# Kernel optimization log

Hardware: AMD Instinct MI355X
Metric: run time of the kernel (lower is better)

Reference implementation:

```python
import jax, jax.numpy as jnp
import numpy as np
import math

C = 256
GROUPS = 8
EPS = 1e-5

def setup_inputs() -> dict:
    key = jax.random.key(0)
    ks = jax.random.split(key, 10)
    b, c, h, w = 4, C, 64, 64
    x = jax.random.normal(ks[0], (b, c, h, w), dtype=jnp.float32)
    scale = 1.0 / math.sqrt(c)
    wq = jax.random.normal(ks[1], (c, c), dtype=jnp.float32) * scale
    wk = jax.random.normal(ks[2], (c, c), dtype=jnp.float32) * scale
    wv = jax.random.normal(ks[3], (c, c), dtype=jnp.float32) * scale
    wp = jax.random.normal(ks[4], (c, c), dtype=jnp.float32) * scale
    bq = jnp.zeros((c,), jnp.float32)
    bk = jnp.zeros((c,), jnp.float32)
    bv = jnp.zeros((c,), jnp.float32)
    bp = jnp.zeros((c,), jnp.float32)
    gamma = jnp.ones((c,), jnp.float32)
    beta = jnp.zeros((c,), jnp.float32)
    return {"x": x, "gamma": gamma, "beta": beta, "wq": wq, "bq": bq,
            "wk": wk, "bk": bk, "wv": wv, "bv": bv, "wp": wp, "bp": bp}

def _group_norm(x, gamma, beta):
    b, c, h, w = x.shape
    xr = x.reshape(b, GROUPS, c // GROUPS, h, w)
    mean = xr.mean(axis=(2, 3, 4), keepdims=True)
    var = xr.var(axis=(2, 3, 4), keepdims=True)
    xn = ((xr - mean) * jax.lax.rsqrt(var + EPS)).reshape(b, c, h, w)
    return xn * gamma[None, :, None, None] + beta[None, :, None, None]

def _conv1x1(x, w, bias):
    # 1x1 conv == channel matmul: [b,c,h,w] x [out,in] -> [b,out,h,w]
    return jnp.einsum('bchw,dc->bdhw', x, w) + bias[None, :, None, None]

def reference(x, gamma, beta, wq, bq, wk, bk, wv, bv, wp, bp):
    b, c, h, w = x.shape
    residual = x
    xn = _group_norm(x, gamma, beta)
    q = _conv1x1(xn, wq, bq).reshape(b, c, h * w).transpose(0, 2, 1)  # [b, hw, c]
    k = _conv1x1(xn, wk, bk).reshape(b, c, h * w)                    # [b, c, hw]
    v = _conv1x1(xn, wv, bv).reshape(b, c, h * w).transpose(0, 2, 1)  # [b, hw, c]
    attn = jnp.einsum('bqc,bck->bqk', q, k) / jnp.sqrt(jnp.float32(c))
    attn = jax.nn.softmax(attn, axis=-1)
    out = jnp.einsum('bqk,bkc->bqc', attn, v)                         # [b, hw, c]
    out = out.transpose(0, 2, 1).reshape(b, c, h, w)
    out = _conv1x1(out, wp, bp)
    return out + residual
```

## Files before the change

### kernel.cpp

```cpp
#include <hip/hip_runtime.h>

#define HW 4096
#define CD 256
#define KB 32
#define NKB 64
#define NSP 2
#define C1 0.09016844f

typedef __bf16 bf16x8v __attribute__((ext_vector_type(8)));
typedef float f32x4 __attribute__((ext_vector_type(4)));
typedef unsigned short u16;
typedef unsigned int u32;
typedef u16 u16x4 __attribute__((ext_vector_type(4)));
typedef u16 u16x8 __attribute__((ext_vector_type(8)));

static __device__ __forceinline__ u16 f2bf(float f){
  __bf16 h = (__bf16)f;
  return __builtin_bit_cast(u16, h);
}
static __device__ __forceinline__ float bf2f(u16 v){
  u32 u = ((u32)v) << 16;
  return __builtin_bit_cast(float, u);
}

static __device__ __forceinline__ f32x4 MFMA(u16x8 a, u16x8 b, f32x4 c){
  return __builtin_amdgcn_mfma_f32_16x16x32_bf16(
      __builtin_bit_cast(bf16x8v, a), __builtin_bit_cast(bf16x8v, b), c, 0, 0, 0);
}

#define GLL16(gsrc, ldst) __builtin_amdgcn_global_load_lds( \
    (const __attribute__((address_space(1))) void*)(gsrc),  \
    (__attribute__((address_space(3))) void*)(ldst), 16, 0, 0)

__global__ void k_prep(const float* __restrict__ wq, const float* __restrict__ wk,
                       const float* __restrict__ wv, const float* __restrict__ wp,
                       u16* __restrict__ Wbf){
  int z = blockIdx.y;
  const float* src = (z==0)?wq:(z==1)?wk:(z==2)?wv:wp;
  int i = (blockIdx.x*256 + threadIdx.x)*4;
  float4 v = *(const float4*)(src + i);
  u16x4 o = { f2bf(v.x), f2bf(v.y), f2bf(v.z), f2bf(v.w) };
  *(u16x4*)(Wbf + z*65536 + i) = o;
}

__global__ void k_gn1(const float* __restrict__ x, float* __restrict__ gpart){
  int g = blockIdx.x, b = blockIdx.y, ck = blockIdx.z;
  int tid = threadIdx.x;
  const float* xp = x + ((size_t)(b*CD) + g*32)*HW + ck*512;
  float s0 = 0.f, s1 = 0.f;
  #pragma unroll
  for (int j = 0; j < 16; ++j){
    int idx = j*1024 + tid*4;
    float4 v = *(const float4*)(xp + (size_t)(idx >> 9)*HW + (idx & 511));
    s0 += v.x + v.y + v.z + v.w;
    s1 += v.x*v.x + v.y*v.y + v.z*v.z + v.w*v.w;
  }
  #pragma unroll
  for (int m = 1; m < 64; m <<= 1){ s0 += __shfl_xor(s0, m); s1 += __shfl_xor(s1, m); }
  __shared__ float red[8];
  int lane = tid & 63, wave = tid >> 6;
  if (lane == 0){ red[wave] = s0; red[4+wave] = s1; }
  __syncthreads();
  if (tid == 0){
    float* dst = gpart + ((b*8 + g)*8 + ck)*2;
    dst[0] = red[0]+red[1]+red[2]+red[3];
    dst[1] = red[4]+red[5]+red[6]+red[7];
  }
}

__global__ void k_gn2(const float* __restrict__ x, const float* __restrict__ gamma,
                      const float* __restrict__ beta, const float* __restrict__ gpart,
                      u16* __restrict__ xnT){
  int g = blockIdx.x, b = blockIdx.y, ck = blockIdx.z;
  int tid = threadIdx.x;
  float s0 = 0.f, s1 = 0.f;
  #pragma unroll
  for (int s = 0; s < 8; ++s){
    const float* p = gpart + ((b*8 + g)*8 + s)*2;
    s0 += p[0]; s1 += p[1];
  }
  float inv_n = 1.0f/(32.0f*HW);
  float mean = s0*inv_n;
  float var = s1*inv_n - mean*mean;
  float rstd = rsqrtf(var + 1e-5f);
  int pl = tid >> 2, c8 = (tid & 3)*8;
  float av[8], bv_[8];
  #pragma unroll
  for (int e = 0; e < 8; ++e){
    int c = g*32 + c8 + e;
    float a = rstd * gamma[c];
    av[e] = a;
    bv_[e] = beta[c] - mean*a;
  }
  const float* xb = x + (size_t)(b*CD + g*32 + c8)*HW;
  #pragma unroll
  for (int it = 0; it < 8; ++it){
    int p = ck*512 + it*64 + pl;
    u16x8 o;
    #pragma unroll
    for (int e = 0; e < 8; ++e){
      float v = xb[(size_t)e*HW + p];
      o[e] = f2bf(v*av[e] + bv_[e]);
    }
    *(u16x8*)(xnT + ((size_t)(b*HW) + p)*CD + g*32 + c8) = o;
  }
}

__global__ __launch_bounds__(256,2) void k_qkv(const u16* __restrict__ xnT, const u16* __restrict__ Wbf,
    const float* __restrict__ bq, const float* __restrict__ bk, const float* __restrict__ bv,
    u16* __restrict__ Q, u16* __restrict__ K, u16* __restrict__ V){
  __shared__ u16 tile[4][4096];
  int z = blockIdx.z, b = blockIdx.y, pbase = blockIdx.x*64;
  int tid = threadIdx.x, lane = tid & 63, wave = tid >> 6;
  int lq = lane & 15, lg = lane >> 4;
  const u16* W = Wbf + z*65536;
  const float* bias = (z==0)?bq:(z==1)?bk:bv;
  int nbase = wave*64;
  f32x4 acc[4][4] = {};
  #pragma unroll
  for (int kk = 0; kk < 8; ++kk){
    u16x8 af[4], bf[4];
    #pragma unroll
    for (int m = 0; m < 4; ++m)
      af[m] = *(const u16x8*)(xnT + ((size_t)(b*HW + pbase + m*16 + lq))*CD + kk*32 + lg*8);
    #pragma unroll
    for (int n = 0; n < 4; ++n)
      bf[n] = *(const u16x8*)(W + (size_t)(nbase + n*16 + lq)*CD + kk*32 + lg*8);
    #pragma unroll
    for (int m = 0; m < 4; ++m)
      #pragma unroll
      for (int n = 0; n < 4; ++n)
        acc[m][n] = MFMA(af[m], bf[n], acc[m][n]);
  }
  #pragma unroll
  for (int n = 0; n < 4; ++n){
    float bb = bias[nbase + n*16 + lq];
    #pragma unroll
    for (int m = 0; m < 4; ++m){
      acc[m][n][0] += bb; acc[m][n][1] += bb; acc[m][n][2] += bb; acc[m][n][3] += bb;
    }
  }
  if (z == 2){
    #pragma unroll
    for (int m = 0; m < 4; ++m)
      #pragma unroll
      for (int n = 0; n < 4; ++n){
        int d = nbase + n*16 + lq;
        int p0 = pbase + m*16 + lg*4;
        u16x4 o = { f2bf(acc[m][n][0]), f2bf(acc[m][n][1]), f2bf(acc[m][n][2]), f2bf(acc[m][n][3]) };
        *(u16x4*)(V + (size_t)(b*CD + d)*HW + p0) = o;
      }
  } else {
    u16* dst = (z==0)?Q:K;
    u16* tl = tile[wave];
    #pragma unroll
    for (int m = 0; m < 4; ++m)
      #pragma unroll
      for (int n = 0; n < 4; ++n)
        #pragma unroll
        for (int r = 0; r < 4; ++r){
          int row = m*16 + lg*4 + r;
          int col = n*16 + lq;
          tl[row*64 + ((((col>>3) + row) & 7)<<3) + (col & 7)] = f2bf(acc[m][n][r]);
        }
    #pragma unroll
    for (int j = 0; j < 8; ++j){
      int idx = j*64 + lane;
      int row = idx >> 3, ch = idx & 7;
      u16x8 v = *(const u16x8*)(tl + row*64 + (((ch + row)&7)<<3));
      *(u16x8*)(dst + ((size_t)(b*HW + pbase + row))*CD + nbase + ch*8) = v;
    }
  }
}

__global__ __launch_bounds__(512,4) void k_attn(const u16* __restrict__ Q, const u16* __restrict__ K,
    const u16* __restrict__ V, u16* __restrict__ Opart, float2* __restrict__ ml){
  extern __shared__ char smem[];
  int tid = threadIdx.x, lane = tid & 63, wave = tid >> 6;
  int lq = lane & 15, lg = lane >> 4;
  int pair = wave >> 1, half = wave & 1;
  int qt = blockIdx.x, sp = blockIdx.y, b = blockIdx.z;
  int qbase = qt*64 + pair*16;
  int key0 = sp*(NKB*KB);

  int ke[2], ve[2];
  #pragma unroll
  for (int i = 0; i < 2; ++i){
    int G = i*512 + tid;
    int kr = G >> 5;
    ke[i] = kr*CD + (((G & 31) ^ kr) & 31)*8;
    int vrow = G >> 3;
    int p = (G >> 2) & 1;
    int j = ((G & 3) - vrow) & 3;
    ve[i] = (vrow*2 + p)*HW + j*8;
  }
  int bvo = (lq>>1)*128 + (((lq&1)*4 + ((lg + (lq>>1)) & 3)))*16;

  u16x8 qa[8];
  #pragma unroll
  for (int cc = 0; cc < 8; ++cc)
    qa[cc] = *(const u16x8*)(Q + ((size_t)(b*HW + qbase + lq))*CD + cc*32 + lg*8);

  f32x4 o[8] = {};
  float m_ = 0.f, l_ = 0.f;

  const u16* Kb = K + (size_t)(b*HW + key0)*CD;
  const u16* Vb = V + (size_t)(b*CD)*HW + key0;
  char* Pw = smem + 65536 + pair*1024;
  float* mb = (float*)(smem + 69632);

  {
    char* kd = smem; char* vd = smem + 32768;
    #pragma unroll
    for (int i = 0; i < 2; ++i){
      GLL16(Kb + ke[i], kd + i*8192 + wave*1024);
      GLL16(Vb + ve[i], vd + i*8192 + wave*1024);
    }
  }
  __syncthreads();
  int cur = 0;
  for (int kb = 0; kb < NKB; ++kb){
    if (kb + 1 < NKB){
      char* kd = smem + (cur^1)*16384;
      const u16* kg = Kb + (size_t)(kb+1)*KB*CD;
      #pragma unroll
      for (int i = 0; i < 2; ++i)
        GLL16(kg + ke[i], kd + i*8192 + wave*1024);
    }
    const char* kt = smem + cur*16384;

    f32x4 sa = (f32x4){0.f,0.f,0.f,0.f};
    int row = half*16 + lq;
    #pragma unroll
    for (int cc = 0; cc < 8; ++cc){
      int ch = cc*4 + lg;
      u16x8 kf = *(const u16x8*)(kt + row*512 + (((ch ^ row) & 31) << 4));
      sa = MFMA(kf, qa[cc], sa);
    }
    float t0 = sa[0]*C1, t1 = sa[1]*C1, t2 = sa[2]*C1, t3 = sa[3]*C1;
    float v = fmaxf(fmaxf(t0, t1), fmaxf(t2, t3));
    v = fmaxf(v, __shfl_xor(v, 16));
    v = fmaxf(v, __shfl_xor(v, 32));
    if (lg == 0) mb[pair*32 + half*16 + lq] = v;
    float rs;
    {
      float p0 = exp2f(t0 - m_), p1 = exp2f(t1 - m_);
      float p2 = exp2f(t2 - m_), p3 = exp2f(t3 - m_);
      rs = (p0 + p1) + (p2 + p3);
      u32 w0 = (u32)f2bf(p0) | ((u32)f2bf(p1) << 16);
      u32 w1 = (u32)f2bf(p2) | ((u32)f2bf(p3) << 16);
      int chunk = 2*half + (lg>>1);
      int slot  = (chunk + (lq>>1)) & 3;
      int base  = (lq>>1)*128 + ((lq&1)*4 + slot)*16;
      *(u32*)(Pw + base + ((2*lg + 0)&3)*4) = w0;
      *(u32*)(Pw + base + ((2*lg + 1)&3)*4) = w1;
    }
    rs += __shfl_xor(rs, 16);
    rs += __shfl_xor(rs, 32);
    l_ += rs;
    if (kb + 1 < NKB){
      asm volatile("s_waitcnt vmcnt(2) lgkmcnt(0)" ::: "memory");
      __builtin_amdgcn_s_barrier();
      __builtin_amdgcn_sched_barrier(0);
      char* vd = smem + 32768 + (cur^1)*16384;
      const u16* vg = Vb + (kb+1)*KB;
      #pragma unroll
      for (int i = 0; i < 2; ++i)
        GLL16(vg + ve[i], vd + i*8192 + wave*1024);
    } else {
      __syncthreads();
    }
    float mx = fmaxf(mb[pair*32 + lq], mb[pair*32 + 16 + lq]);
    u16x8 pa = *(const u16x8*)(Pw + bvo);
    const char* vt = smem + 32768 + cur*16384;
    #pragma unroll
    for (int f = 0; f < 8; ++f){
      u16x8 vf = *(const u16x8*)(vt + (half*8 + f)*1024 + bvo);
      o[f] = MFMA(pa, vf, o[f]);
    }
    if (!__all(mx <= m_ + 8.0f)){
      float nm = fmaxf(m_, mx);
      float corr = exp2f(m_ - nm);
      m_ = nm;
      l_ *= corr;
      float cr[4];
      #pragma unroll
      for (int r = 0; r < 4; ++r)
        cr[r] = __shfl(corr, lg*4 + r);
      #pragma unroll
      for (int f = 0; f < 8; ++f)
        #pragma unroll
        for (int r = 0; r < 4; ++r)
          o[f][r] *= cr[r];
    }
    cur ^= 1;
  }
  __syncthreads();
  if (lg == 0) mb[pair*32 + half*16 + lq] = l_;
  __syncthreads();
  float l_tot = mb[pair*32 + lq] + mb[pair*32 + 16 + lq];
  size_t ob = ((size_t)((sp*4 + b)*HW + qbase))*CD;
  #pragma unroll
  for (int f = 0; f < 8; ++f){
    int c = (half*8 + f)*16 + lq;
    #pragma unroll
    for (int r = 0; r < 4; ++r)
      Opart[ob + (size_t)(lg*4 + r)*CD + c] = f2bf(o[f][r]);
  }
  if (half == 0 && lg == 0)
    ml[(size_t)(sp*4 + b)*HW + qbase + lq] = make_float2(m_, l_tot);
}

__global__ void k_comb(const u16* __restrict__ Opart, const float2* __restrict__ ml,
                       u16* __restrict__ Opm){
  int b = blockIdx.y;
  int q = blockIdx.x*8 + (threadIdx.x >> 5);
  int c0 = (threadIdx.x & 31)*8;
  float2 e[NSP];
  float m = -3.0e38f;
  #pragma unroll
  for (int s = 0; s < NSP; ++s){
    e[s] = ml[(size_t)(s*4 + b)*HW + q];
    m = fmaxf(m, e[s].x);
  }
  float w[NSP], den = 0.f;
  #pragma unroll
  for (int s = 0; s < NSP; ++s){
    w[s] = exp2f(e[s].x - m);
    den += e[s].y * w[s];
  }
  float inv = 1.0f / den;
  float sum[8] = {};
  #pragma unroll
  for (int s = 0; s < NSP; ++s){
    u16x8 v = *(const u16x8*)(Opart + ((size_t)((s*4 + b)*HW) + q)*CD + c0);
    float ws = w[s];
    #pragma unroll
    for (int t = 0; t < 8; ++t)
      sum[t] += bf2f(v[t]) * ws;
  }
  u16x8 o;
  #pragma unroll
  for (int t = 0; t < 8; ++t)
    o[t] = f2bf(sum[t]*inv);
  *(u16x8*)(Opm + ((size_t)(b*HW) + q)*CD + c0) = o;
}

__global__ __launch_bounds__(256,2) void k_proj(const u16* __restrict__ Opm, const u16* __restrict__ Wp,
    const float* __restrict__ bp, const float* __restrict__ x, float* __restrict__ out){
  int b = blockIdx.y, pbase = blockIdx.x*64;
  int tid = threadIdx.x, lane = tid & 63, wave = tid >> 6;
  int lq = lane & 15, lg = lane >> 4;
  int nbase = wave*64;
  f32x4 acc[4][4] = {};
  #pragma unroll
  for (int kk = 0; kk < 8; ++kk){
    u16x8 af[4], bf[4];
    #pragma unroll
    for (int m = 0; m < 4; ++m)
      af[m] = *(const u16x8*)(Opm + ((size_t)(b*HW + pbase + m*16 + lq))*CD + kk*32 + lg*8);
    #pragma unroll
    for (int n = 0; n < 4; ++n)
      bf[n] = *(const u16x8*)(Wp + (size_t)(nbase + n*16 + lq)*CD + kk*32 + lg*8);
    #pragma unroll
    for (int m = 0; m < 4; ++m)
      #pragma unroll
      for (int n = 0; n < 4; ++n)
        acc[m][n] = MFMA(af[m], bf[n], acc[m][n]);
  }
  #pragma unroll
  for (int m = 0; m < 4; ++m)
    #pragma unroll
    for (int n = 0; n < 4; ++n){
      int d = nbase + n*16 + lq;
      int p0 = pbase + m*16 + lg*4;
      size_t base = (size_t)(b*CD + d)*HW + p0;
      float bb = bp[d];
      float4 res = *(const float4*)(x + base);
      float4 ov;
      ov.x = acc[m][n][0] + bb + res.x;
      ov.y = acc[m][n][1] + bb + res.y;
      ov.z = acc[m][n][2] + bb + res.z;
      ov.w = acc[m][n][3] + bb + res.w;
      *(float4*)(out + base) = ov;
    }
}

extern "C" void kernel_launch(void* const* d_in, const int* in_sizes, int n_in,
                              void* d_out, int out_size, void* d_ws, size_t ws_size,
                              hipStream_t stream){
  const float* x     = (const float*)d_in[0];
  const float* gamma = (const float*)d_in[1];
  const float* beta  = (const float*)d_in[2];
  const float* wq    = (const float*)d_in[3];
  const float* bq    = (const float*)d_in[4];
  const float* wk    = (const float*)d_in[5];
  const float* bk    = (const float*)d_in[6];
  const float* wv    = (const float*)d_in[7];
  const float* bv    = (const float*)d_in[8];
  const float* wp    = (const float*)d_in[9];
  const float* bp    = (const float*)d_in[10];
  float* out = (float*)d_out;

  char* ws = (char*)d_ws;
  u16*   xnT   = (u16*)(ws);
  u16*   Qb    = (u16*)(ws + (8ull<<20));
  u16*   Kb    = (u16*)(ws + (16ull<<20));
  u16*   Vb    = (u16*)(ws + (24ull<<20));
  u16*   Opm   = (u16*)(ws + (32ull<<20));
  u16*   Wbf   = (u16*)(ws + (40ull<<20));
  float2* mlb  = (float2*)(ws + (40ull<<20) + (512ull<<10));
  u16*   Opart = (u16*)(ws + (41ull<<20));
  float* gpart = (float*)Qb;

  hipFuncSetAttribute((const void*)k_attn, hipFuncAttributeMaxDynamicSharedMemorySize, 70144);

  k_prep<<<dim3(64,4), 256, 0, stream>>>(wq, wk, wv, wp, Wbf);
  k_gn1 <<<dim3(8,4,8), 256, 0, stream>>>(x, gpart);
  k_gn2 <<<dim3(8,4,8), 256, 0, stream>>>(x, gamma, beta, gpart, xnT);
  k_qkv <<<dim3(64,4,3), 256, 0, stream>>>(xnT, Wbf, bq, bk, bv, Qb, Kb, Vb);
  k_attn<<<dim3(64,NSP,4), 512, 70144, stream>>>(Qb, Kb, Vb, Opart, mlb);
  k_comb<<<dim3(512,4), 256, 0, stream>>>(Opart, mlb, Opm);
  k_proj<<<dim3(64,4), 256, 0, stream>>>(Opm, Wbf + 3*65536, bp, x, out);
}
```

Baseline: 164.9 us.

## Fuse weight prep into GN stats, prescale Q, rebarrier attention loop, halve proj tile

The weight bf16 conversion moves into the group-norm statistics kernel, which removes one kernel launch. The softmax scale C1 is folded into Q when Q is produced, so the attention loop no longer multiplies each score. The attention loop's barriers are rearranged: an unconditional wait and barrier before the V prefetch, plus a second barrier at the end of each iteration. The projection kernel uses 32-row tiles, doubling its grid to 512 blocks so more CUs have work. The extra barrier per iteration could add stall time, and bf16 rounding of the prescaled Q changes numerics slightly.

```diff
diff --git a/kernel.cpp b/kernel.cpp
--- a/kernel.cpp
+++ b/kernel.cpp
@@ -32,20 +32,21 @@
     (const __attribute__((address_space(1))) void*)(gsrc),  \
     (__attribute__((address_space(3))) void*)(ldst), 16, 0, 0)
 
-__global__ void k_prep(const float* __restrict__ wq, const float* __restrict__ wk,
-                       const float* __restrict__ wv, const float* __restrict__ wp,
-                       u16* __restrict__ Wbf){
-  int z = blockIdx.y;
-  const float* src = (z==0)?wq:(z==1)?wk:(z==2)?wv:wp;
-  int i = (blockIdx.x*256 + threadIdx.x)*4;
-  float4 v = *(const float4*)(src + i);
-  u16x4 o = { f2bf(v.x), f2bf(v.y), f2bf(v.z), f2bf(v.w) };
-  *(u16x4*)(Wbf + z*65536 + i) = o;
-}
-
-__global__ void k_gn1(const float* __restrict__ x, float* __restrict__ gpart){
+__global__ void k_gn1(const float* __restrict__ x,
+                      const float* __restrict__ wq, const float* __restrict__ wk,
+                      const float* __restrict__ wv, const float* __restrict__ wp,
+                      u16* __restrict__ Wbf, float* __restrict__ gpart){
   int g = blockIdx.x, b = blockIdx.y, ck = blockIdx.z;
   int tid = threadIdx.x;
+  {
+    int bid = (ck*4 + b)*8 + g;
+    int i4 = bid*1024 + tid*4;
+    int z = i4 >> 16, off = i4 & 65535;
+    const float* src = (z==0)?wq:(z==1)?wk:(z==2)?wv:wp;
+    float4 v = *(const float4*)(src + off);
+    u16x4 o = { f2bf(v.x), f2bf(v.y), f2bf(v.z), f2bf(v.w) };
+    *(u16x4*)(Wbf + i4) = o;
+  }
   const float* xp = x + ((size_t)(b*CD) + g*32)*HW + ck*512;
   float s0 = 0.f, s1 = 0.f;
   #pragma unroll
@@ -115,6 +116,7 @@
   int lq = lane & 15, lg = lane >> 4;
   const u16* W = Wbf + z*65536;
   const float* bias = (z==0)?bq:(z==1)?bk:bv;
+  float scl = (z==0) ? C1 : 1.0f;
   int nbase = wave*64;
   f32x4 acc[4][4] = {};
   #pragma unroll
@@ -136,9 +138,10 @@
   for (int n = 0; n < 4; ++n){
     float bb = bias[nbase + n*16 + lq];
     #pragma unroll
-    for (int m = 0; m < 4; ++m){
-      acc[m][n][0] += bb; acc[m][n][1] += bb; acc[m][n][2] += bb; acc[m][n][3] += bb;
-    }
+    for (int m = 0; m < 4; ++m)
+      #pragma unroll
+      for (int r = 0; r < 4; ++r)
+        acc[m][n][r] = (acc[m][n][r] + bb) * scl;
   }
   if (z == 2){
     #pragma unroll
@@ -237,15 +240,14 @@
       u16x8 kf = *(const u16x8*)(kt + row*512 + (((ch ^ row) & 31) << 4));
       sa = MFMA(kf, qa[cc], sa);
     }
-    float t0 = sa[0]*C1, t1 = sa[1]*C1, t2 = sa[2]*C1, t3 = sa[3]*C1;
-    float v = fmaxf(fmaxf(t0, t1), fmaxf(t2, t3));
+    float v = fmaxf(fmaxf(sa[0], sa[1]), fmaxf(sa[2], sa[3]));
     v = fmaxf(v, __shfl_xor(v, 16));
     v = fmaxf(v, __shfl_xor(v, 32));
     if (lg == 0) mb[pair*32 + half*16 + lq] = v;
     float rs;
     {
-      float p0 = exp2f(t0 - m_), p1 = exp2f(t1 - m_);
-      float p2 = exp2f(t2 - m_), p3 = exp2f(t3 - m_);
+      float p0 = exp2f(sa[0] - m_), p1 = exp2f(sa[1] - m_);
+      float p2 = exp2f(sa[2] - m_), p3 = exp2f(sa[3] - m_);
       rs = (p0 + p1) + (p2 + p3);
       u32 w0 = (u32)f2bf(p0) | ((u32)f2bf(p1) << 16);
       u32 w1 = (u32)f2bf(p2) | ((u32)f2bf(p3) << 16);
@@ -258,17 +260,19 @@
     rs += __shfl_xor(rs, 16);
     rs += __shfl_xor(rs, 32);
     l_ += rs;
+    if (kb + 1 < NKB)
+      asm volatile("s_waitcnt vmcnt(2) lgkmcnt(0)" ::: "memory");
+    else
+      asm volatile("s_waitcnt vmcnt(0) lgkmcnt(0)" ::: "memory");
+    __builtin_amdgcn_s_barrier();
+    __builtin_amdgcn_sched_barrier(0);
+
     if (kb + 1 < NKB){
-      asm volatile("s_waitcnt vmcnt(2) lgkmcnt(0)" ::: "memory");
-      __builtin_amdgcn_s_barrier();
-      __builtin_amdgcn_sched_barrier(0);
       char* vd = smem + 32768 + (cur^1)*16384;
       const u16* vg = Vb + (kb+1)*KB;
       #pragma unroll
       for (int i = 0; i < 2; ++i)
         GLL16(vg + ve[i], vd + i*8192 + wave*1024);
-    } else {
-      __syncthreads();
     }
     float mx = fmaxf(mb[pair*32 + lq], mb[pair*32 + 16 + lq]);
     u16x8 pa = *(const u16x8*)(Pw + bvo);
@@ -292,6 +296,11 @@
         #pragma unroll
         for (int r = 0; r < 4; ++r)
           o[f][r] *= cr[r];
+    }
+    if (kb + 1 < NKB){
+      asm volatile("s_waitcnt vmcnt(2)" ::: "memory");
+      __builtin_amdgcn_s_barrier();
+      __builtin_amdgcn_sched_barrier(0);
     }
     cur ^= 1;
   }
@@ -348,28 +357,28 @@
 
 __global__ __launch_bounds__(256,2) void k_proj(const u16* __restrict__ Opm, const u16* __restrict__ Wp,
     const float* __restrict__ bp, const float* __restrict__ x, float* __restrict__ out){
-  int b = blockIdx.y, pbase = blockIdx.x*64;
+  int b = blockIdx.y, pbase = blockIdx.x*32;
   int tid = threadIdx.x, lane = tid & 63, wave = tid >> 6;
   int lq = lane & 15, lg = lane >> 4;
   int nbase = wave*64;
-  f32x4 acc[4][4] = {};
+  f32x4 acc[2][4] = {};
   #pragma unroll
   for (int kk = 0; kk < 8; ++kk){
-    u16x8 af[4], bf[4];
-    #pragma unroll
-    for (int m = 0; m < 4; ++m)
+    u16x8 af[2], bf[4];
+    #pragma unroll
+    for (int m = 0; m < 2; ++m)
       af[m] = *(const u16x8*)(Opm + ((size_t)(b*HW + pbase + m*16 + lq))*CD + kk*32 + lg*8);
     #pragma unroll
     for (int n = 0; n < 4; ++n)
       bf[n] = *(const u16x8*)(Wp + (size_t)(nbase + n*16 + lq)*CD + kk*32 + lg*8);
     #pragma unroll
-    for (int m = 0; m < 4; ++m)
+    for (int m = 0; m < 2; ++m)
       #pragma unroll
       for (int n = 0; n < 4; ++n)
         acc[m][n] = MFMA(af[m], bf[n], acc[m][n]);
   }
   #pragma unroll
-  for (int m = 0; m < 4; ++m)
+  for (int m = 0; m < 2; ++m)
     #pragma unroll
     for (int n = 0; n < 4; ++n){
       int d = nbase + n*16 + lq;
@@ -415,11 +424,10 @@
 
   hipFuncSetAttribute((const void*)k_attn, hipFuncAttributeMaxDynamicSharedMemorySize, 70144);
 
-  k_prep<<<dim3(64,4), 256, 0, stream>>>(wq, wk, wv, wp, Wbf);
-  k_gn1 <<<dim3(8,4,8), 256, 0, stream>>>(x, gpart);
+  k_gn1 <<<dim3(8,4,8), 256, 0, stream>>>(x, wq, wk, wv, wp, Wbf, gpart);
   k_gn2 <<<dim3(8,4,8), 256, 0, stream>>>(x, gamma, beta, gpart, xnT);
   k_qkv <<<dim3(64,4,3), 256, 0, stream>>>(xnT, Wbf, bq, bk, bv, Qb, Kb, Vb);
   k_attn<<<dim3(64,NSP,4), 512, 70144, stream>>>(Qb, Kb, Vb, Opart, mlb);
   k_comb<<<dim3(512,4), 256, 0, stream>>>(Opart, mlb, Opm);
-  k_proj<<<dim3(64,4), 256, 0, stream>>>(Opm, Wbf + 3*65536, bp, x, out);
-}
+  k_proj<<<dim3(128,4), 256, 0, stream>>>(Opm, Wbf + 3*65536, bp, x, out);
+}
```

Result: no change. 163.0 us (-1.2%).
